# Kernel optimization log

Hardware: AMD Instinct MI355X
Metric: run time of the kernel (lower is better)

Reference implementation:

```python
import jax, jax.numpy as jnp
import numpy as np

NUM_HEADS = 8
EPS = 1e-12  # tf.nn.l2_normalize epsilon


def _l2_normalize(t):
    # tf.nn.l2_normalize: x * rsqrt(max(sum(x^2), eps)) along last axis
    sq = jnp.sum(t * t, axis=-1, keepdims=True)
    return t * jax.lax.rsqrt(jnp.maximum(sq, EPS))


def setup_inputs() -> dict:
    key = jax.random.key(0)
    ks = jax.random.split(key, 4)
    B, N, C = 8, 4096, 512
    x = jax.random.normal(ks[0], (B, N, C), dtype=jnp.float32)
    w_qkv = jax.random.normal(ks[1], (C, 3 * C), dtype=jnp.float32) * (C ** -0.5)
    b_qkv = jnp.zeros((3 * C,), dtype=jnp.float32)
    w_proj = jax.random.normal(ks[2], (C, C), dtype=jnp.float32) * (C ** -0.5)
    b_proj = jnp.zeros((C,), dtype=jnp.float32)
    return {"x": x, "w_qkv": w_qkv, "b_qkv": b_qkv, "w_proj": w_proj, "b_proj": b_proj}


def reference(x, w_qkv, b_qkv, w_proj, b_proj):
    B, N, C = x.shape
    h = NUM_HEADS
    d = C // h
    scale = d ** -0.5
    qkv = x @ w_qkv + b_qkv                        # [B,N,3C]
    qkv = qkv.reshape(B, N, 3, h, d)
    qkv = jnp.transpose(qkv, (2, 0, 3, 1, 4))      # [3,B,h,N,d]
    q, k, v = qkv[0], qkv[1], qkv[2]
    q = _l2_normalize(q) * scale
    k = _l2_normalize(k)
    # channel-wise attention: q^T k over tokens -> [B,h,d,d]
    attn = jnp.einsum('bhnd,bhne->bhde', q, k)
    attn = jax.nn.softmax(attn, axis=-1)
    out = jnp.einsum('bhnd,bhde->bhne', v, attn)   # [B,h,N,d]
    out = jnp.transpose(out, (0, 2, 1, 3)).reshape(B, N, C)
    out = out @ w_proj + b_proj
    return out
```

## Files before the change

### kernel.cpp

```cpp
#include <hip/hip_runtime.h>
#include <stdint.h>

#define NB 8
#define NN 4096
#define NC 512
#define NH 8
#define ATTN_CH 16

typedef __bf16 bf16x8 __attribute__((ext_vector_type(8)));
typedef float floatx4 __attribute__((ext_vector_type(4)));

__device__ __forceinline__ unsigned short f2bf(float f) {
  union { float f; unsigned u; } v; v.f = f;
  return (unsigned short)((v.u + 0x7fffu + ((v.u >> 16) & 1u)) >> 16);
}
__device__ __forceinline__ float2 bfp2f(unsigned u) {
  union { unsigned x; float f; } lo, hi;
  lo.x = u << 16; hi.x = u & 0xffff0000u;
  return make_float2(lo.f, hi.f);
}

__device__ __forceinline__ void async_ld16(void* lds, const void* g) {
  auto* gp = (const __attribute__((address_space(1))) unsigned int*)(uintptr_t)g;
  auto* lp = (__attribute__((address_space(3))) unsigned int*)(uintptr_t)lds;
  __builtin_amdgcn_global_load_lds(gp, lp, 16, 0, 0);
}

__global__ __launch_bounds__(256) void k_prep(const float* __restrict__ x,
                                              unsigned short* __restrict__ xb,
                                              const float* __restrict__ w,
                                              unsigned short* __restrict__ wt) {
  int bid = blockIdx.x;
  if (bid < 16384) {
    int i = (bid * 256 + threadIdx.x) * 4;
    float4 v = *(const float4*)(x + i);
    ushort4 o;
    o.x = f2bf(v.x); o.y = f2bf(v.y); o.z = f2bf(v.z); o.w = f2bf(v.w);
    *(ushort4*)(xb + i) = o;
    return;
  }
  __shared__ float tile[64][65];
  int b2 = bid - 16384;
  int nn0 = (b2 % 24) * 64, kk0 = (b2 / 24) * 64;
  int t = threadIdx.x;
#pragma unroll
  for (int i = 0; i < 16; i++) {
    int id = t + i * 256;
    int r = id >> 6, c = id & 63;
    tile[c][r] = w[(size_t)(kk0 + r) * 1536 + nn0 + c];
  }
  __syncthreads();
#pragma unroll
  for (int i = 0; i < 16; i++) {
    int id = t + i * 256;
    int rn = id >> 6, ck = id & 63;
    wt[(size_t)(nn0 + rn) * 512 + kk0 + ck] = f2bf(tile[rn][ck]);
  }
}

__global__ __launch_bounds__(512, 2) void k_gemm_qkv(const unsigned short* __restrict__ A,
                                                     const unsigned short* __restrict__ Bt,
                                                     const float* __restrict__ bias,
                                                     unsigned short* __restrict__ Cq) {
  const int LDA = 512, LDB = 512, LDC = 1536;
  int bid = blockIdx.x;
  int xcd = bid & 7, local = bid >> 3;
  int mloc = local / 6, nt = local - mloc * 6;
  int m0 = (xcd * 16 + mloc) * 256, n0 = nt * 256;

  int tid = threadIdx.x;
  int lane = tid & 63, w = tid >> 6;
  int wrb = (w >> 2) * 128;
  int wcb = (w & 3) * 64;
  int quad = lane >> 4, rr = lane & 15;
  int r8 = lane >> 3, cg = lane & 7;
  int cgs8 = (cg ^ r8) * 8;
  const int swz = rr & 7;
  int w8 = w * 8;

  __shared__ __align__(16) unsigned short As[2][256 * 64];
  __shared__ __align__(16) unsigned short Bs[2][256 * 64];

  floatx4 acc[8][4];
#pragma unroll
  for (int i = 0; i < 8; i++)
#pragma unroll
    for (int j = 0; j < 4; j++) acc[i][j] = (floatx4){0.f, 0.f, 0.f, 0.f};

  auto stage = [&](int ss, int kt) {
    int k0 = kt << 6;
#pragma unroll
    for (int i = 0; i < 4; i++) {
      int rb = i * 64 + w8;
      async_ld16(&As[ss][rb * 64], A + (size_t)(m0 + rb + r8) * LDA + k0 + cgs8);
      async_ld16(&Bs[ss][rb * 64], Bt + (size_t)(n0 + rb + r8) * LDB + k0 + cgs8);
    }
  };

  auto compute = [&](int ss) {
#pragma unroll
    for (int kk = 0; kk < 2; kk++) {
      int ksl = (((kk << 2) + quad) ^ swz) << 3;
      bf16x8 af[8];
#pragma unroll
      for (int mi = 0; mi < 8; mi++)
        af[mi] = *(const bf16x8*)&As[ss][(wrb + mi * 16 + rr) * 64 + ksl];
      bf16x8 bf[2];
#pragma unroll
      for (int ni = 0; ni < 2; ni++)
        bf[ni] = *(const bf16x8*)&Bs[ss][(wcb + ni * 16 + rr) * 64 + ksl];
      __builtin_amdgcn_s_setprio(1);
#pragma unroll
      for (int mi = 0; mi < 8; mi++)
#pragma unroll
        for (int ni = 0; ni < 2; ni++)
          acc[mi][ni] = __builtin_amdgcn_mfma_f32_16x16x32_bf16(af[mi], bf[ni], acc[mi][ni], 0, 0, 0);
      __builtin_amdgcn_s_setprio(0);
#pragma unroll
      for (int ni = 0; ni < 2; ni++)
        bf[ni] = *(const bf16x8*)&Bs[ss][(wcb + (ni + 2) * 16 + rr) * 64 + ksl];
      __builtin_amdgcn_s_setprio(1);
#pragma unroll
      for (int mi = 0; mi < 8; mi++)
#pragma unroll
        for (int ni = 0; ni < 2; ni++)
          acc[mi][ni + 2] = __builtin_amdgcn_mfma_f32_16x16x32_bf16(af[mi], bf[ni], acc[mi][ni + 2], 0, 0, 0);
      __builtin_amdgcn_s_setprio(0);
    }
  };

  stage(0, 0);
  stage(1, 1);
#pragma unroll 1
  for (int t = 0; t < 8; t++) {
    if (t < 7) asm volatile("s_waitcnt vmcnt(8)" ::: "memory");
    else       asm volatile("s_waitcnt vmcnt(0)" ::: "memory");
    __builtin_amdgcn_s_barrier();
    __builtin_amdgcn_sched_barrier(0);
    compute(t & 1);
    __builtin_amdgcn_sched_barrier(0);
    __builtin_amdgcn_s_barrier();
    if (t < 6) stage(t & 1, t + 2);
  }

#pragma unroll
  for (int ni = 0; ni < 4; ni++) {
    int col = n0 + wcb + ni * 16 + rr;
    float bv = bias[col];
#pragma unroll
    for (int mi = 0; mi < 8; mi++) {
      int rbase = m0 + wrb + mi * 16 + quad * 4;
#pragma unroll
      for (int r = 0; r < 4; r++)
        Cq[(size_t)(rbase + r) * LDC + col] = f2bf(acc[mi][ni][r] + bv);
    }
  }
}

__global__ __launch_bounds__(256) void k_attn(const unsigned short* __restrict__ QKV,
                                              float* __restrict__ logits_p) {
  int chunk = blockIdx.x, hh = blockIdx.y, b = blockIdx.z;
  int tid = threadIdx.x, w = tid >> 6, l = tid & 63;
  int quad = l >> 4, rr = l & 15;

  __shared__ __align__(16) unsigned char smem[40960];
  unsigned short* qT = (unsigned short*)smem + w * 5120;
  unsigned short* kT = qT + 2560;
  float* ps = (float*)smem;

  floatx4 acc[4][4];
#pragma unroll
  for (int i = 0; i < 4; i++)
#pragma unroll
    for (int j = 0; j < 4; j++) acc[i][j] = (floatx4){0.f, 0.f, 0.f, 0.f};

  int tok8 = l >> 3;
  int seg = l & 7;
  int sw = seg & 3;

  for (int s = 0; s < 2; s++) {
    int nbase = chunk * 256 + w * 64 + s * 32;
#pragma unroll
    for (int c = 0; c < 4; c++) {
      int n = nbase + c * 8 + tok8;
      const unsigned short* p = QKV + (size_t)(b * 4096 + n) * 1536 + hh * 64 + seg * 8;
      uint4 vq = *(const uint4*)p;
      uint4 vk = *(const uint4*)(p + 512);
      unsigned uq[4] = {vq.x, vq.y, vq.z, vq.w};
      unsigned uk[4] = {vk.x, vk.y, vk.z, vk.w};
      float qf[8], kf[8], sq = 0.f, sk = 0.f;
#pragma unroll
      for (int e = 0; e < 4; e++) {
        float2 f = bfp2f(uq[e]); qf[2 * e] = f.x; qf[2 * e + 1] = f.y; sq += f.x * f.x + f.y * f.y;
        float2 g = bfp2f(uk[e]); kf[2 * e] = g.x; kf[2 * e + 1] = g.y; sk += g.x * g.x + g.y * g.y;
      }
      sq += __shfl_xor(sq, 1); sq += __shfl_xor(sq, 2); sq += __shfl_xor(sq, 4);
      sk += __shfl_xor(sk, 1); sk += __shfl_xor(sk, 2); sk += __shfl_xor(sk, 4);
      float scq = 0.125f * rsqrtf(fmaxf(sq, 1e-12f));
      float sck = rsqrtf(fmaxf(sk, 1e-12f));
      int col = ((c ^ sw) << 3) + tok8;
#pragma unroll
      for (int j = 0; j < 8; j++) {
        int dim = seg * 8 + j;
        qT[dim * 40 + col] = f2bf(qf[j] * scq);
        kT[dim * 40 + col] = f2bf(kf[j] * sck);
      }
    }
    bf16x8 af[4], bfr[4];
#pragma unroll
    for (int mi = 0; mi < 4; mi++) {
      int s3 = (mi * 2 + (rr >> 3)) & 3;
      int off = (mi * 16 + rr) * 40 + ((quad ^ s3) << 3);
      af[mi] = *(const bf16x8*)(qT + off);
      bfr[mi] = *(const bf16x8*)(kT + off);
    }
#pragma unroll
    for (int mi = 0; mi < 4; mi++)
#pragma unroll
      for (int ni = 0; ni < 4; ni++)
        acc[mi][ni] = __builtin_amdgcn_mfma_f32_16x16x32_bf16(af[mi], bfr[ni], acc[mi][ni], 0, 0, 0);
  }

  __syncthreads();
  for (int r2 = 0; r2 < 4; r2++) {
    if (w == r2) {
#pragma unroll
      for (int mi = 0; mi < 4; mi++)
#pragma unroll
        for (int ni = 0; ni < 4; ni++)
#pragma unroll
          for (int r = 0; r < 4; r++) {
            int d = mi * 16 + quad * 4 + r, e = ni * 16 + rr;
            if (r2 == 0) ps[d * 64 + e] = acc[mi][ni][r];
            else         ps[d * 64 + e] += acc[mi][ni][r];
          }
    }
    __syncthreads();
  }
  float* outp = logits_p + ((size_t)(b * 8 + hh) * ATTN_CH + chunk) * 4096;
  for (int i = tid; i < 4096; i += 256) outp[i] = ps[i];
}

__global__ __launch_bounds__(256) void k_softmax_m(const float* __restrict__ logits_p,
                                                   const float* __restrict__ wproj,
                                                   unsigned short* __restrict__ Mt) {
  int cc = blockIdx.x & 3, rh = blockIdx.x >> 2;
  int hh = blockIdx.y, b = blockIdx.z;
  int t = threadIdx.x;
  __shared__ float ls[32][64];
  __shared__ float red[32][8];
  __shared__ float inv[32];
  const float* lp = logits_p + (size_t)((b * 8 + hh) * ATTN_CH) * 4096 + rh * 2048;
#pragma unroll
  for (int i = 0; i < 8; i++) {
    int id = t + i * 256;
    float s = 0.f;
#pragma unroll
    for (int c = 0; c < ATTN_CH; c++) s += lp[c * 4096 + id];
    ls[id >> 6][id & 63] = s;
  }
  __syncthreads();
  int row = t >> 3, part = t & 7;
  float mx = -1e30f;
#pragma unroll
  for (int j = 0; j < 8; j++) mx = fmaxf(mx, ls[row][part * 8 + j]);
  red[row][part] = mx;
  __syncthreads();
  if (part == 0) {
    float m2 = red[row][0];
#pragma unroll
    for (int j = 1; j < 8; j++) m2 = fmaxf(m2, red[row][j]);
    inv[row] = m2;
  }
  __syncthreads();
  float rm = inv[row];
  float s = 0.f;
#pragma unroll
  for (int j = 0; j < 8; j++) {
    float e = __expf(ls[row][part * 8 + j] - rm);
    ls[row][part * 8 + j] = e;
    s += e;
  }
  red[row][part] = s;
  __syncthreads();
  if (part == 0) {
    float s2 = 0.f;
#pragma unroll
    for (int j = 0; j < 8; j++) s2 += red[row][j];
    inv[row] = 1.0f / s2;
  }
  __syncthreads();

  int cout = cc * 128 + (t & 127);
  int half = t >> 7;
  float wreg[64];
#pragma unroll
  for (int ee = 0; ee < 64; ee++) wreg[ee] = wproj[(size_t)(hh * 64 + ee) * 512 + cout];
  unsigned short ob[16];
#pragma unroll
  for (int d2 = 0; d2 < 16; d2++) {
    int dd = half * 16 + d2;
    float a = 0.f;
#pragma unroll
    for (int e4 = 0; e4 < 16; e4++) {
      float4 p4 = *(const float4*)&ls[dd][e4 * 4];
      a += p4.x * wreg[e4 * 4] + p4.y * wreg[e4 * 4 + 1] + p4.z * wreg[e4 * 4 + 2] + p4.w * wreg[e4 * 4 + 3];
    }
    ob[d2] = f2bf(a * inv[dd]);
  }
  uint4* dst = (uint4*)(Mt + ((size_t)(b * 512 + cout)) * 512 + hh * 64 + rh * 32 + half * 16);
  dst[0] = ((const uint4*)ob)[0];
  dst[1] = ((const uint4*)ob)[1];
}

__global__ __launch_bounds__(512, 2) void k_gemm_out(const unsigned short* __restrict__ QKV,
                                                     const unsigned short* __restrict__ MtAll,
                                                     const float* __restrict__ bias,
                                                     float* __restrict__ Out) {
  const int LDA = 1536, LDB = 512, LDC = 512;
  int bid = blockIdx.x;
  int xcd = bid & 7, local = bid >> 3;
  int gid = xcd * 32 + local;
  int b = gid >> 5;
  int id = gid & 31;
  int m0 = (id >> 1) * 256;
  int n0 = (id & 1) * 256;
  const unsigned short* A = QKV + (size_t)b * NN * 1536 + 1024;
  const unsigned short* Bt = MtAll + (size_t)b * 512 * 512;

  int tid = threadIdx.x;
  int lane = tid & 63, w = tid >> 6;
  int wrb = (w >> 2) * 128;
  int wcb = (w & 3) * 64;
  int quad = lane >> 4, rr = lane & 15;
  int r8 = lane >> 3, cg = lane & 7;
  int cgs8 = (cg ^ r8) * 8;
  const int swz = rr & 7;
  int w8 = w * 8;

  __shared__ __align__(16) unsigned short As[2][256 * 64];
  __shared__ __align__(16) unsigned short Bs[2][256 * 64];

  floatx4 acc[8][4];
#pragma unroll
  for (int i = 0; i < 8; i++)
#pragma unroll
    for (int j = 0; j < 4; j++) acc[i][j] = (floatx4){0.f, 0.f, 0.f, 0.f};

  auto stage = [&](int ss, int kt) {
    int k0 = kt << 6;
#pragma unroll
    for (int i = 0; i < 4; i++) {
      int rb = i * 64 + w8;
      async_ld16(&As[ss][rb * 64], A + (size_t)(m0 + rb + r8) * LDA + k0 + cgs8);
      async_ld16(&Bs[ss][rb * 64], Bt + (size_t)(n0 + rb + r8) * LDB + k0 + cgs8);
    }
  };

  auto compute = [&](int ss) {
#pragma unroll
    for (int kk = 0; kk < 2; kk++) {
      int ksl = (((kk << 2) + quad) ^ swz) << 3;
      bf16x8 af[8];
#pragma unroll
      for (int mi = 0; mi < 8; mi++)
        af[mi] = *(const bf16x8*)&As[ss][(wrb + mi * 16 + rr) * 64 + ksl];
      bf16x8 bf[2];
#pragma unroll
      for (int ni = 0; ni < 2; ni++)
        bf[ni] = *(const bf16x8*)&Bs[ss][(wcb + ni * 16 + rr) * 64 + ksl];
      __builtin_amdgcn_s_setprio(1);
#pragma unroll
      for (int mi = 0; mi < 8; mi++)
#pragma unroll
        for (int ni = 0; ni < 2; ni++)
          acc[mi][ni] = __builtin_amdgcn_mfma_f32_16x16x32_bf16(af[mi], bf[ni], acc[mi][ni], 0, 0, 0);
      __builtin_amdgcn_s_setprio(0);
#pragma unroll
      for (int ni = 0; ni < 2; ni++)
        bf[ni] = *(const bf16x8*)&Bs[ss][(wcb + (ni + 2) * 16 + rr) * 64 + ksl];
      __builtin_amdgcn_s_setprio(1);
#pragma unroll
      for (int mi = 0; mi < 8; mi++)
#pragma unroll
        for (int ni = 0; ni < 2; ni++)
          acc[mi][ni + 2] = __builtin_amdgcn_mfma_f32_16x16x32_bf16(af[mi], bf[ni], acc[mi][ni + 2], 0, 0, 0);
      __builtin_amdgcn_s_setprio(0);
    }
  };

  stage(0, 0);
  stage(1, 1);
#pragma unroll 1
  for (int t = 0; t < 8; t++) {
    if (t < 7) asm volatile("s_waitcnt vmcnt(8)" ::: "memory");
    else       asm volatile("s_waitcnt vmcnt(0)" ::: "memory");
    __builtin_amdgcn_s_barrier();
    __builtin_amdgcn_sched_barrier(0);
    compute(t & 1);
    __builtin_amdgcn_sched_barrier(0);
    __builtin_amdgcn_s_barrier();
    if (t < 6) stage(t & 1, t + 2);
  }

#pragma unroll
  for (int ni = 0; ni < 4; ni++) {
    int col = n0 + wcb + ni * 16 + rr;
    float bv = bias[col];
#pragma unroll
    for (int mi = 0; mi < 8; mi++) {
      int rbase = m0 + wrb + mi * 16 + quad * 4;
#pragma unroll
      for (int r = 0; r < 4; r++)
        Out[(size_t)b * NN * LDC + (size_t)(rbase + r) * LDC + col] = acc[mi][ni][r] + bv;
    }
  }
}

extern "C" void kernel_launch(void* const* d_in, const int* in_sizes, int n_in,
                              void* d_out, int out_size, void* d_ws, size_t ws_size,
                              hipStream_t stream) {
  const float* x      = (const float*)d_in[0];
  const float* w_qkv  = (const float*)d_in[1];
  const float* b_qkv  = (const float*)d_in[2];
  const float* w_proj = (const float*)d_in[3];
  const float* b_proj = (const float*)d_in[4];
  float* out = (float*)d_out;

  char* ws = (char*)d_ws;
  size_t off = 0;
  auto alloc = [&](size_t bytes) -> void* {
    void* p = ws + off;
    off += (bytes + 255) & ~(size_t)255;
    return p;
  };
  unsigned short* xb       = (unsigned short*)alloc((size_t)NB * NN * NC * 2);
  unsigned short* wT       = (unsigned short*)alloc((size_t)1536 * 512 * 2);
  unsigned short* qkvb     = (unsigned short*)alloc((size_t)NB * NN * 3 * NC * 2);
  float*          logits_p = (float*)alloc((size_t)NB * NH * ATTN_CH * 4096 * 4);
  unsigned short* Mt       = (unsigned short*)alloc((size_t)NB * 512 * 512 * 2);

  k_prep<<<16576, 256, 0, stream>>>(x, xb, w_qkv, wT);
  k_gemm_qkv<<<768, 512, 0, stream>>>(xb, wT, b_qkv, qkvb);
  k_attn<<<dim3(ATTN_CH, 8, 8), 256, 0, stream>>>(qkvb, logits_p);
  k_softmax_m<<<dim3(8, 8, 8), 256, 0, stream>>>(logits_p, w_proj, Mt);
  k_gemm_out<<<256, 512, 0, stream>>>(qkvb, Mt, b_proj, out);
}
```

Measured before the change: 287.5 us.

## Restructure GEMM pipelines with triple-buffered A, early prefetch and quadrant MFMA ordering

```diff
diff --git a/kernel.cpp b/kernel.cpp
--- a/kernel.cpp
+++ b/kernel.cpp
@@ -72,14 +72,17 @@
   int lane = tid & 63, w = tid >> 6;
   int wrb = (w >> 2) * 128;
   int wcb = (w & 3) * 64;
+  int ah = w >> 2;
+  int bh = (w & 3) >> 1;
+  int brow0 = (w & 1) * 64;
   int quad = lane >> 4, rr = lane & 15;
+  int swz = rr & 7;
   int r8 = lane >> 3, cg = lane & 7;
   int cgs8 = (cg ^ r8) * 8;
-  const int swz = rr & 7;
   int w8 = w * 8;
 
-  __shared__ __align__(16) unsigned short As[2][256 * 64];
-  __shared__ __align__(16) unsigned short Bs[2][256 * 64];
+  __shared__ __align__(16) unsigned short Als[3][2][128 * 64];
+  __shared__ __align__(16) unsigned short Bls[2][2][128 * 64];
 
   floatx4 acc[8][4];
 #pragma unroll
@@ -87,60 +90,71 @@
 #pragma unroll
     for (int j = 0; j < 4; j++) acc[i][j] = (floatx4){0.f, 0.f, 0.f, 0.f};
 
-  auto stage = [&](int ss, int kt) {
+  auto stageA = [&](int ss, int h, int kt) {
     int k0 = kt << 6;
-#pragma unroll
-    for (int i = 0; i < 4; i++) {
+    const unsigned short* src = A + (size_t)(m0 + h * 128) * LDA + k0 + cgs8;
+#pragma unroll
+    for (int i = 0; i < 2; i++) {
       int rb = i * 64 + w8;
-      async_ld16(&As[ss][rb * 64], A + (size_t)(m0 + rb + r8) * LDA + k0 + cgs8);
-      async_ld16(&Bs[ss][rb * 64], Bt + (size_t)(n0 + rb + r8) * LDB + k0 + cgs8);
-    }
-  };
-
-  auto compute = [&](int ss) {
-#pragma unroll
-    for (int kk = 0; kk < 2; kk++) {
-      int ksl = (((kk << 2) + quad) ^ swz) << 3;
-      bf16x8 af[8];
-#pragma unroll
-      for (int mi = 0; mi < 8; mi++)
-        af[mi] = *(const bf16x8*)&As[ss][(wrb + mi * 16 + rr) * 64 + ksl];
-      bf16x8 bf[2];
+      async_ld16(&Als[ss][h][rb * 64], src + (size_t)(rb + r8) * LDA);
+    }
+  };
+  auto stageB = [&](int ss, int h, int kt) {
+    int k0 = kt << 6;
+    const unsigned short* src = Bt + (size_t)(n0 + h * 128) * LDB + k0 + cgs8;
+#pragma unroll
+    for (int i = 0; i < 2; i++) {
+      int rb = i * 64 + w8;
+      async_ld16(&Bls[ss][h][rb * 64], src + (size_t)(rb + r8) * LDB);
+    }
+  };
+  auto rdA = [&](int ss, int mi, int s) -> bf16x8 {
+    return *(const bf16x8*)&Als[ss][ah][(mi * 16 + rr) * 64 + (((s * 4 + quad) ^ swz)) * 8];
+  };
+  auto rdB = [&](int ss, int ni, int s) -> bf16x8 {
+    return *(const bf16x8*)&Bls[ss][bh][(brow0 + ni * 16 + rr) * 64 + (((s * 4 + quad) ^ swz)) * 8];
+  };
+  auto mfmaQ = [&](bf16x8 (&af)[4][2], bf16x8 (&bf)[2][2], int mo, int no) {
+    __builtin_amdgcn_s_setprio(1);
+#pragma unroll
+    for (int mi = 0; mi < 4; mi++)
 #pragma unroll
       for (int ni = 0; ni < 2; ni++)
-        bf[ni] = *(const bf16x8*)&Bs[ss][(wcb + ni * 16 + rr) * 64 + ksl];
-      __builtin_amdgcn_s_setprio(1);
-#pragma unroll
-      for (int mi = 0; mi < 8; mi++)
-#pragma unroll
-        for (int ni = 0; ni < 2; ni++)
-          acc[mi][ni] = __builtin_amdgcn_mfma_f32_16x16x32_bf16(af[mi], bf[ni], acc[mi][ni], 0, 0, 0);
-      __builtin_amdgcn_s_setprio(0);
-#pragma unroll
-      for (int ni = 0; ni < 2; ni++)
-        bf[ni] = *(const bf16x8*)&Bs[ss][(wcb + (ni + 2) * 16 + rr) * 64 + ksl];
-      __builtin_amdgcn_s_setprio(1);
-#pragma unroll
-      for (int mi = 0; mi < 8; mi++)
-#pragma unroll
-        for (int ni = 0; ni < 2; ni++)
-          acc[mi][ni + 2] = __builtin_amdgcn_mfma_f32_16x16x32_bf16(af[mi], bf[ni], acc[mi][ni + 2], 0, 0, 0);
-      __builtin_amdgcn_s_setprio(0);
-    }
-  };
-
-  stage(0, 0);
-  stage(1, 1);
+#pragma unroll
+        for (int s = 0; s < 2; s++)
+          acc[mo + mi][no + ni] = __builtin_amdgcn_mfma_f32_16x16x32_bf16(af[mi][s], bf[ni][s], acc[mo + mi][no + ni], 0, 0, 0);
+    __builtin_amdgcn_s_setprio(0);
+  };
+
+  stageA(0, 0, 0); stageA(0, 1, 0);
+  stageB(0, 0, 0); stageB(0, 1, 0);
+  stageA(1, 0, 1); stageA(1, 1, 1);
+
 #pragma unroll 1
-  for (int t = 0; t < 8; t++) {
-    if (t < 7) asm volatile("s_waitcnt vmcnt(8)" ::: "memory");
+  for (int k = 0; k < 8; k++) {
+    int sa = k % 3, sb = k & 1;
+    if (k < 7) asm volatile("s_waitcnt vmcnt(4)" ::: "memory");
     else       asm volatile("s_waitcnt vmcnt(0)" ::: "memory");
-    __builtin_amdgcn_s_barrier();
+    asm volatile("s_barrier" ::: "memory");
+    if (k < 7) { stageB((k + 1) & 1, 0, k + 1); stageB((k + 1) & 1, 1, k + 1); }
+    if (k < 6) { int ss = (k + 2) % 3; stageA(ss, 0, k + 2); stageA(ss, 1, k + 2); }
     __builtin_amdgcn_sched_barrier(0);
-    compute(t & 1);
-    __builtin_amdgcn_sched_barrier(0);
-    __builtin_amdgcn_s_barrier();
-    if (t < 6) stage(t & 1, t + 2);
+
+    bf16x8 afA[4][2], afB[4][2], bfA[2][2], bfB[2][2];
+#pragma unroll
+    for (int mi = 0; mi < 4; mi++) { afA[mi][0] = rdA(sa, mi, 0); afA[mi][1] = rdA(sa, mi, 1); }
+#pragma unroll
+    for (int ni = 0; ni < 2; ni++) { bfA[ni][0] = rdB(sb, ni, 0); bfA[ni][1] = rdB(sb, ni, 1); }
+    mfmaQ(afA, bfA, 0, 0);
+#pragma unroll
+    for (int ni = 0; ni < 2; ni++) { bfB[ni][0] = rdB(sb, 2 + ni, 0); bfB[ni][1] = rdB(sb, 2 + ni, 1); }
+    mfmaQ(afA, bfB, 0, 2);
+#pragma unroll
+    for (int mi = 0; mi < 4; mi++) { afB[mi][0] = rdA(sa, 4 + mi, 0); afB[mi][1] = rdA(sa, 4 + mi, 1); }
+    mfmaQ(afB, bfB, 4, 2);
+#pragma unroll
+    for (int ni = 0; ni < 2; ni++) { bfA[ni][0] = rdB(sb, ni, 0); bfA[ni][1] = rdB(sb, ni, 1); }
+    mfmaQ(afB, bfA, 4, 0);
   }
 
 #pragma unroll
@@ -320,11 +334,9 @@
   const int LDA = 1536, LDB = 512, LDC = 512;
   int bid = blockIdx.x;
   int xcd = bid & 7, local = bid >> 3;
-  int gid = xcd * 32 + local;
-  int b = gid >> 5;
-  int id = gid & 31;
-  int m0 = (id >> 1) * 256;
-  int n0 = (id & 1) * 256;
+  int b = xcd;
+  int mloc = local >> 1, nt = local & 1;
+  int m0 = mloc * 256, n0 = nt * 256;
   const unsigned short* A = QKV + (size_t)b * NN * 1536 + 1024;
   const unsigned short* Bt = MtAll + (size_t)b * 512 * 512;
 
@@ -332,14 +344,17 @@
   int lane = tid & 63, w = tid >> 6;
   int wrb = (w >> 2) * 128;
   int wcb = (w & 3) * 64;
+  int ah = w >> 2;
+  int bh = (w & 3) >> 1;
+  int brow0 = (w & 1) * 64;
   int quad = lane >> 4, rr = lane & 15;
+  int swz = rr & 7;
   int r8 = lane >> 3, cg = lane & 7;
   int cgs8 = (cg ^ r8) * 8;
-  const int swz = rr & 7;
   int w8 = w * 8;
 
-  __shared__ __align__(16) unsigned short As[2][256 * 64];
-  __shared__ __align__(16) unsigned short Bs[2][256 * 64];
+  __shared__ __align__(16) unsigned short Als[3][2][128 * 64];
+  __shared__ __align__(16) unsigned short Bls[2][2][128 * 64];
 
   floatx4 acc[8][4];
 #pragma unroll
@@ -347,60 +362,71 @@
 #pragma unroll
     for (int j = 0; j < 4; j++) acc[i][j] = (floatx4){0.f, 0.f, 0.f, 0.f};
 
-  auto stage = [&](int ss, int kt) {
+  auto stageA = [&](int ss, int h, int kt) {
     int k0 = kt << 6;
-#pragma unroll
-    for (int i = 0; i < 4; i++) {
+    const unsigned short* src = A + (size_t)(m0 + h * 128) * LDA + k0 + cgs8;
+#pragma unroll
+    for (int i = 0; i < 2; i++) {
       int rb = i * 64 + w8;
-      async_ld16(&As[ss][rb * 64], A + (size_t)(m0 + rb + r8) * LDA + k0 + cgs8);
-      async_ld16(&Bs[ss][rb * 64], Bt + (size_t)(n0 + rb + r8) * LDB + k0 + cgs8);
-    }
-  };
-
-  auto compute = [&](int ss) {
-#pragma unroll
-    for (int kk = 0; kk < 2; kk++) {
-      int ksl = (((kk << 2) + quad) ^ swz) << 3;
-      bf16x8 af[8];
-#pragma unroll
-      for (int mi = 0; mi < 8; mi++)
-        af[mi] = *(const bf16x8*)&As[ss][(wrb + mi * 16 + rr) * 64 + ksl];
-      bf16x8 bf[2];
+      async_ld16(&Als[ss][h][rb * 64], src + (size_t)(rb + r8) * LDA);
+    }
+  };
+  auto stageB = [&](int ss, int h, int kt) {
+    int k0 = kt << 6;
+    const unsigned short* src = Bt + (size_t)(n0 + h * 128) * LDB + k0 + cgs8;
+#pragma unroll
+    for (int i = 0; i < 2; i++) {
+      int rb = i * 64 + w8;
+      async_ld16(&Bls[ss][h][rb * 64], src + (size_t)(rb + r8) * LDB);
+    }
+  };
+  auto rdA = [&](int ss, int mi, int s) -> bf16x8 {
+    return *(const bf16x8*)&Als[ss][ah][(mi * 16 + rr) * 64 + (((s * 4 + quad) ^ swz)) * 8];
+  };
+  auto rdB = [&](int ss, int ni, int s) -> bf16x8 {
+    return *(const bf16x8*)&Bls[ss][bh][(brow0 + ni * 16 + rr) * 64 + (((s * 4 + quad) ^ swz)) * 8];
+  };
+  auto mfmaQ = [&](bf16x8 (&af)[4][2], bf16x8 (&bf)[2][2], int mo, int no) {
+    __builtin_amdgcn_s_setprio(1);
+#pragma unroll
+    for (int mi = 0; mi < 4; mi++)
 #pragma unroll
       for (int ni = 0; ni < 2; ni++)
-        bf[ni] = *(const bf16x8*)&Bs[ss][(wcb + ni * 16 + rr) * 64 + ksl];
-      __builtin_amdgcn_s_setprio(1);
-#pragma unroll
-      for (int mi = 0; mi < 8; mi++)
-#pragma unroll
-        for (int ni = 0; ni < 2; ni++)
-          acc[mi][ni] = __builtin_amdgcn_mfma_f32_16x16x32_bf16(af[mi], bf[ni], acc[mi][ni], 0, 0, 0);
-      __builtin_amdgcn_s_setprio(0);
-#pragma unroll
-      for (int ni = 0; ni < 2; ni++)
-        bf[ni] = *(const bf16x8*)&Bs[ss][(wcb + (ni + 2) * 16 + rr) * 64 + ksl];
-      __builtin_amdgcn_s_setprio(1);
-#pragma unroll
-      for (int mi = 0; mi < 8; mi++)
-#pragma unroll
-        for (int ni = 0; ni < 2; ni++)
-          acc[mi][ni + 2] = __builtin_amdgcn_mfma_f32_16x16x32_bf16(af[mi], bf[ni], acc[mi][ni + 2], 0, 0, 0);
-      __builtin_amdgcn_s_setprio(0);
-    }
-  };
-
-  stage(0, 0);
-  stage(1, 1);
+#pragma unroll
+        for (int s = 0; s < 2; s++)
+          acc[mo + mi][no + ni] = __builtin_amdgcn_mfma_f32_16x16x32_bf16(af[mi][s], bf[ni][s], acc[mo + mi][no + ni], 0, 0, 0);
+    __builtin_amdgcn_s_setprio(0);
+  };
+
+  stageA(0, 0, 0); stageA(0, 1, 0);
+  stageB(0, 0, 0); stageB(0, 1, 0);
+  stageA(1, 0, 1); stageA(1, 1, 1);
+
 #pragma unroll 1
-  for (int t = 0; t < 8; t++) {
-    if (t < 7) asm volatile("s_waitcnt vmcnt(8)" ::: "memory");
+  for (int k = 0; k < 8; k++) {
+    int sa = k % 3, sb = k & 1;
+    if (k < 7) asm volatile("s_waitcnt vmcnt(4)" ::: "memory");
     else       asm volatile("s_waitcnt vmcnt(0)" ::: "memory");
-    __builtin_amdgcn_s_barrier();
+    asm volatile("s_barrier" ::: "memory");
+    if (k < 7) { stageB((k + 1) & 1, 0, k + 1); stageB((k + 1) & 1, 1, k + 1); }
+    if (k < 6) { int ss = (k + 2) % 3; stageA(ss, 0, k + 2); stageA(ss, 1, k + 2); }
     __builtin_amdgcn_sched_barrier(0);
-    compute(t & 1);
-    __builtin_amdgcn_sched_barrier(0);
-    __builtin_amdgcn_s_barrier();
-    if (t < 6) stage(t & 1, t + 2);
+
+    bf16x8 afA[4][2], afB[4][2], bfA[2][2], bfB[2][2];
+#pragma unroll
+    for (int mi = 0; mi < 4; mi++) { afA[mi][0] = rdA(sa, mi, 0); afA[mi][1] = rdA(sa, mi, 1); }
+#pragma unroll
+    for (int ni = 0; ni < 2; ni++) { bfA[ni][0] = rdB(sb, ni, 0); bfA[ni][1] = rdB(sb, ni, 1); }
+    mfmaQ(afA, bfA, 0, 0);
+#pragma unroll
+    for (int ni = 0; ni < 2; ni++) { bfB[ni][0] = rdB(sb, 2 + ni, 0); bfB[ni][1] = rdB(sb, 2 + ni, 1); }
+    mfmaQ(afA, bfB, 0, 2);
+#pragma unroll
+    for (int mi = 0; mi < 4; mi++) { afB[mi][0] = rdA(sa, 4 + mi, 0); afB[mi][1] = rdA(sa, 4 + mi, 1); }
+    mfmaQ(afB, bfB, 4, 2);
+#pragma unroll
+    for (int ni = 0; ni < 2; ni++) { bfA[ni][0] = rdB(sb, ni, 0); bfA[ni][1] = rdB(sb, ni, 1); }
+    mfmaQ(afB, bfA, 4, 0);
   }
 
 #pragma unroll
```

After: 283.7 us. About the same (-1.3%).
